# Optimization experiments

Measured on AMD Instinct MI355X. Metric: run time of the kernel, lower is better.

The kernel has to match this reference:

```python
import jax, jax.numpy as jnp
import numpy as np

B, L, E, H, A = 32, 4096, 512, 512, 256


def setup_inputs() -> dict:
    key = jax.random.key(0)
    ks = jax.random.split(key, 8)
    s_e = 1.0 / np.sqrt(E)
    s_h = 1.0 / np.sqrt(H)
    s_a = 1.0 / np.sqrt(A)
    return {
        "features": jax.random.normal(ks[0], (B, L, E), jnp.float32),
        "decoder_hidden": jax.random.normal(ks[1], (B, H), jnp.float32),
        "W_enc": jax.random.uniform(ks[2], (E, A), jnp.float32, -s_e, s_e),
        "b_enc": jax.random.uniform(ks[3], (A,), jnp.float32, -s_e, s_e),
        "W_dec": jax.random.uniform(ks[4], (H, A), jnp.float32, -s_h, s_h),
        "b_dec": jax.random.uniform(ks[5], (A,), jnp.float32, -s_h, s_h),
        "W_v": jax.random.uniform(ks[6], (A, 1), jnp.float32, -s_a, s_a),
        "b_v": jax.random.uniform(ks[7], (1,), jnp.float32, -s_a, s_a),
    }


def reference(features, decoder_hidden, W_enc, b_enc, W_dec, b_dec, W_v, b_v):
    # encoder/decoder projections
    enc_attn = jnp.einsum("ble,ea->bla", features, W_enc) + b_enc  # [B,L,A]
    dec_attn = decoder_hidden @ W_dec + b_dec                       # [B,A]
    sim = jax.nn.relu(enc_attn + dec_attn[:, None, :])              # [B,L,A]
    scores = (jnp.einsum("bla,ao->blo", sim, W_v) + b_v)[..., 0]    # [B,L]
    attn_weights = jax.nn.softmax(scores, axis=1)                   # [B,L]
    output = jnp.einsum("ble,bl->be", features, attn_weights)       # [B,E]
    return output, attn_weights
```

## Files before the change

kernel.cpp:

```cpp
#include <hip/hip_runtime.h>
#include <hip/hip_bf16.h>
#include <stdint.h>


typedef __attribute__((ext_vector_type(8))) short bf16x8;
typedef __attribute__((ext_vector_type(4))) float f32x4;

__device__ __forceinline__ unsigned short f32_to_bf16(float f) {
    union { float f; unsigned u; } v; v.f = f;
    unsigned u = v.u;
    u += 0x7fffu + ((u >> 16) & 1u);
    return (unsigned short)(u >> 16);
}

__device__ __forceinline__ void async_load16(const void* g, void* l) {
    __builtin_amdgcn_global_load_lds(
        (const __attribute__((address_space(1))) unsigned int*)g,
        (__attribute__((address_space(3))) unsigned int*)l, 16, 0, 0);
}

__global__ __launch_bounds__(256) void prep_kernel(
    const float* __restrict__ dh, const float* __restrict__ W_enc,
    const float* __restrict__ b_enc, const float* __restrict__ W_dec,
    const float* __restrict__ b_dec, unsigned short* __restrict__ Wp,
    float* __restrict__ dec_full, unsigned* __restrict__ cnt)
{
    int t = threadIdx.x;
    if (blockIdx.x < 32) {
        int b = blockIdx.x;
        if (b == 0 && t < 32) cnt[t] = 0;
        __shared__ float dhs[512];
        dhs[t]       = dh[b * 512 + t];
        dhs[t + 256] = dh[b * 512 + 256 + t];
        __syncthreads();
        float a0 = 0.f, a1 = 0.f, a2 = 0.f, a3 = 0.f;
        float a4 = 0.f, a5 = 0.f, a6 = 0.f, a7 = 0.f;
        #pragma unroll 4
        for (int h = 0; h < 512; h += 8) {
            a0 += dhs[h + 0] * W_dec[(h + 0) * 256 + t];
            a1 += dhs[h + 1] * W_dec[(h + 1) * 256 + t];
            a2 += dhs[h + 2] * W_dec[(h + 2) * 256 + t];
            a3 += dhs[h + 3] * W_dec[(h + 3) * 256 + t];
            a4 += dhs[h + 4] * W_dec[(h + 4) * 256 + t];
            a5 += dhs[h + 5] * W_dec[(h + 5) * 256 + t];
            a6 += dhs[h + 6] * W_dec[(h + 6) * 256 + t];
            a7 += dhs[h + 7] * W_dec[(h + 7) * 256 + t];
        }
        dec_full[b * 256 + t] =
            ((a0 + a1) + (a2 + a3)) + ((a4 + a5) + (a6 + a7)) + b_enc[t] + b_dec[t];
    } else {
        int tid = (blockIdx.x - 32) * 256 + t;
        #pragma unroll
        for (int i = 0; i < 8; ++i) {
            int d = tid + i * 16384;
            int j = d & 7;
            int n = (d >> 3) & 255;
            int chunk = (d >> 11) & 7;
            int kb = d >> 14;
            int k = kb * 64 + chunk * 8 + j;
            Wp[d] = f32_to_bf16(W_enc[k * 256 + n]);
        }
    }
}

__global__ __launch_bounds__(256, 2) void score_kernel(
    const float* __restrict__ feat, const unsigned short* __restrict__ Wp,
    const float* __restrict__ dec_full, const float* __restrict__ W_v,
    float* __restrict__ scores, float* __restrict__ m_c,
    float* __restrict__ o_part, unsigned* __restrict__ cnt,
    float* __restrict__ out)
{
    __shared__ unsigned short Alds[8192];
    __shared__ unsigned short Blds[16384];
    __shared__ float red[4][128];
    __shared__ float sblk[128];
    __shared__ float wexp[128];
    __shared__ float mshr;
    __shared__ float red2x[128], red2y[128], red2z[128], red2w[128];
    __shared__ unsigned dflag;

    const int t = threadIdx.x;
    const int lane = t & 63;
    const int wave = t >> 6;
    const int r0 = blockIdx.x * 128;
    const int b = r0 >> 12;

    float wv[4], dec[4];
    #pragma unroll
    for (int ct = 0; ct < 4; ++ct) {
        int a = wave * 64 + ct * 16 + (lane & 15);
        wv[ct] = W_v[a];
        dec[ct] = dec_full[b * 256 + a];
    }

    f32x4 acc[8][4];
    #pragma unroll
    for (int mt = 0; mt < 8; ++mt)
        #pragma unroll
        for (int ct = 0; ct < 4; ++ct)
            acc[mt][ct] = f32x4{0.f, 0.f, 0.f, 0.f};

    float4 av[8];
    #pragma unroll
    for (int it = 0; it < 8; ++it) {
        int lin = it * 256 + t;
        int m = lin >> 4, kq = lin & 15;
        av[it] = *(const float4*)(feat + (size_t)(r0 + m) * 512 + kq * 4);
    }

    for (int ks = 0; ks < 8; ++ks) {
        #pragma unroll
        for (int q = 0; q < 8; ++q) {
            int c = q * 256 + wave * 64 + lane;
            async_load16(Wp + ks * 16384 + c * 8, Blds + c * 8);
        }
        #pragma unroll
        for (int it = 0; it < 8; ++it) {
            int lin = it * 256 + t;
            int m = lin >> 4, kq = lin & 15;
            ushort4 w;
            w.x = f32_to_bf16(av[it].x);
            w.y = f32_to_bf16(av[it].y);
            w.z = f32_to_bf16(av[it].z);
            w.w = f32_to_bf16(av[it].w);
            int chunk = kq >> 1, jh = kq & 1;
            *(ushort4*)(Alds + m * 64 + ((chunk ^ (m & 7)) * 8) + jh * 4) = w;
        }
        __syncthreads();
        if (ks < 7) {
            #pragma unroll
            for (int it = 0; it < 8; ++it) {
                int lin = it * 256 + t;
                int m = lin >> 4, kq = lin & 15;
                av[it] = *(const float4*)(feat + (size_t)(r0 + m) * 512 + (ks + 1) * 64 + kq * 4);
            }
        }
        #pragma unroll
        for (int kk = 0; kk < 2; ++kk) {
            int chunk = kk * 4 + (lane >> 4);
            bf16x8 bfr[4];
            #pragma unroll
            for (int ct = 0; ct < 4; ++ct) {
                int n = wave * 64 + ct * 16 + (lane & 15);
                bfr[ct] = *(const bf16x8*)(Blds + (chunk * 256 + n) * 8);
            }
            #pragma unroll
            for (int mt = 0; mt < 8; ++mt) {
                int m = mt * 16 + (lane & 15);
                bf16x8 afr = *(const bf16x8*)(Alds + m * 64 + ((chunk ^ (m & 7)) * 8));
                #pragma unroll
                for (int ct = 0; ct < 4; ++ct)
                    acc[mt][ct] = __builtin_amdgcn_mfma_f32_16x16x32_bf16(
                        afr, bfr[ct], acc[mt][ct], 0, 0, 0);
            }
        }
        __syncthreads();
    }

    #pragma unroll
    for (int mt = 0; mt < 8; ++mt) {
        #pragma unroll
        for (int r = 0; r < 4; ++r) {
            float p = 0.f;
            #pragma unroll
            for (int ct = 0; ct < 4; ++ct) {
                float v = acc[mt][ct][r] + dec[ct];
                v = v > 0.f ? v : 0.f;
                p += v * wv[ct];
            }
            p += __shfl_xor(p, 1);
            p += __shfl_xor(p, 2);
            p += __shfl_xor(p, 4);
            p += __shfl_xor(p, 8);
            if ((lane & 15) == 0)
                red[wave][mt * 16 + (lane >> 4) * 4 + r] = p;
        }
    }
    __syncthreads();
    if (t < 128) {
        float v = red[0][t] + red[1][t] + red[2][t] + red[3][t];
        sblk[t] = v;
        scores[r0 + t] = v;
    }
    __syncthreads();
    if (t < 64) {
        float m = fmaxf(sblk[t], sblk[t + 64]);
        #pragma unroll
        for (int o = 1; o < 64; o <<= 1) m = fmaxf(m, __shfl_xor(m, o));
        if (t == 0) mshr = m;
    }
    __syncthreads();
    float mb = mshr;
    if (t < 128) wexp[t] = __expf(sblk[t] - mb);
    __syncthreads();

    int e4 = t & 127, lh = t >> 7;
    float ax = 0.f, ay = 0.f, az = 0.f, aw = 0.f;
    #pragma unroll 8
    for (int i = 0; i < 64; ++i) {
        int l = i * 2 + lh;
        float wl = wexp[l];
        const float4 f = *(const float4*)(feat + (size_t)(r0 + l) * 512 + e4 * 4);
        ax += wl * f.x; ay += wl * f.y; az += wl * f.z; aw += wl * f.w;
    }
    if (lh) { red2x[e4] = ax; red2y[e4] = ay; red2z[e4] = az; red2w[e4] = aw; }
    __syncthreads();
    if (!lh) {
        float4 r;
        r.x = ax + red2x[e4]; r.y = ay + red2y[e4];
        r.z = az + red2z[e4]; r.w = aw + red2w[e4];
        *(float4*)(o_part + (size_t)blockIdx.x * 512 + e4 * 4) = r;
        if (t == 0) m_c[blockIdx.x] = mb;
    }

    __syncthreads();
    if (t == 0) {
        unsigned old = __hip_atomic_fetch_add(cnt + b, 1u,
                                              __ATOMIC_ACQ_REL,
                                              __HIP_MEMORY_SCOPE_AGENT);
        dflag = (old == 31u) ? 1u : 0u;
    }
    __syncthreads();
    if (!dflag) return;

    const float* s = scores + b * 4096;
    float vals[16];
    float m = -1e30f;
    #pragma unroll
    for (int i = 0; i < 16; ++i) { vals[i] = s[t + i * 256]; m = fmaxf(m, vals[i]); }
    #pragma unroll
    for (int o = 1; o < 64; o <<= 1) m = fmaxf(m, __shfl_xor(m, o));
    if ((t & 63) == 0) red[0][t >> 6] = m;
    __syncthreads();
    m = fmaxf(fmaxf(red[0][0], red[0][1]), fmaxf(red[0][2], red[0][3]));

    float z = 0.f;
    #pragma unroll
    for (int i = 0; i < 16; ++i) { vals[i] = __expf(vals[i] - m); z += vals[i]; }
    #pragma unroll
    for (int o = 1; o < 64; o <<= 1) z += __shfl_xor(z, o);
    if ((t & 63) == 0) red[1][t >> 6] = z;
    __syncthreads();
    z = red[1][0] + red[1][1] + red[1][2] + red[1][3];
    float invz = 1.f / z;
    #pragma unroll
    for (int i = 0; i < 16; ++i)
        out[16384 + b * 4096 + t + i * 256] = vals[i] * invz;

    if (t < 32) red[2][t] = __expf(m_c[b * 32 + t] - m) * invz;
    __syncthreads();
    float a0 = 0.f, a1 = 0.f;
    #pragma unroll 8
    for (int c = 0; c < 32; ++c) {
        const float2 v = *(const float2*)(o_part + (size_t)(b * 32 + c) * 512 + t * 2);
        a0 += red[2][c] * v.x; a1 += red[2][c] * v.y;
    }
    float2 r2; r2.x = a0; r2.y = a1;
    *(float2*)(out + b * 512 + t * 2) = r2;
}

extern "C" void kernel_launch(void* const* d_in, const int* in_sizes, int n_in,
                              void* d_out, int out_size, void* d_ws, size_t ws_size,
                              hipStream_t stream) {
    const float* feat  = (const float*)d_in[0];
    const float* dh    = (const float*)d_in[1];
    const float* W_enc = (const float*)d_in[2];
    const float* b_enc = (const float*)d_in[3];
    const float* W_dec = (const float*)d_in[4];
    const float* b_dec = (const float*)d_in[5];
    const float* W_v   = (const float*)d_in[6];

    unsigned short* Wp = (unsigned short*)d_ws;
    float* dec_full = (float*)((char*)d_ws + 262144);
    float* scores   = (float*)((char*)d_ws + 294912);
    float* m_c      = (float*)((char*)d_ws + 819200);
    unsigned* cnt   = (unsigned*)((char*)d_ws + 823296);
    float* o_part   = (float*)((char*)d_ws + 1048576);
    float* out      = (float*)d_out;

    prep_kernel<<<96, 256, 0, stream>>>(dh, W_enc, b_enc, W_dec, b_dec, Wp, dec_full, cnt);
    score_kernel<<<1024, 256, 0, stream>>>(feat, Wp, dec_full, W_v, scores, m_c,
                                           o_part, cnt, out);
}
```

Measured before the change: 461.2 us.

## Halve row tile, read B fragments from global, double-buffer A in LDS

New measurement: 522.2 us. 13.2% more time.

```diff
diff --git a/kernel.cpp b/kernel.cpp
--- a/kernel.cpp
+++ b/kernel.cpp
@@ -11,12 +11,6 @@
     unsigned u = v.u;
     u += 0x7fffu + ((u >> 16) & 1u);
     return (unsigned short)(u >> 16);
-}
-
-__device__ __forceinline__ void async_load16(const void* g, void* l) {
-    __builtin_amdgcn_global_load_lds(
-        (const __attribute__((address_space(1))) unsigned int*)g,
-        (__attribute__((address_space(3))) unsigned int*)l, 16, 0, 0);
 }
 
 __global__ __launch_bounds__(256) void prep_kernel(
@@ -63,18 +57,17 @@
     }
 }
 
-__global__ __launch_bounds__(256, 2) void score_kernel(
+__global__ __launch_bounds__(256, 3) void score_kernel(
     const float* __restrict__ feat, const unsigned short* __restrict__ Wp,
     const float* __restrict__ dec_full, const float* __restrict__ W_v,
     float* __restrict__ scores, float* __restrict__ m_c,
     float* __restrict__ o_part, unsigned* __restrict__ cnt,
     float* __restrict__ out)
 {
-    __shared__ unsigned short Alds[8192];
-    __shared__ unsigned short Blds[16384];
-    __shared__ float red[4][128];
-    __shared__ float sblk[128];
-    __shared__ float wexp[128];
+    __shared__ __align__(16) unsigned short Alds[2][4096];
+    __shared__ float red[4][64];
+    __shared__ float sblk[64];
+    __shared__ float wexp[64];
     __shared__ float mshr;
     __shared__ float red2x[128], red2y[128], red2z[128], red2w[128];
     __shared__ unsigned dflag;
@@ -82,7 +75,7 @@
     const int t = threadIdx.x;
     const int lane = t & 63;
     const int wave = t >> 6;
-    const int r0 = blockIdx.x * 128;
+    const int r0 = blockIdx.x * 64;
     const int b = r0 >> 12;
 
     float wv[4], dec[4];
@@ -93,48 +86,45 @@
         dec[ct] = dec_full[b * 256 + a];
     }
 
-    f32x4 acc[8][4];
-    #pragma unroll
-    for (int mt = 0; mt < 8; ++mt)
+    f32x4 acc[4][4];
+    #pragma unroll
+    for (int mt = 0; mt < 4; ++mt)
         #pragma unroll
         for (int ct = 0; ct < 4; ++ct)
             acc[mt][ct] = f32x4{0.f, 0.f, 0.f, 0.f};
 
-    float4 av[8];
-    #pragma unroll
-    for (int it = 0; it < 8; ++it) {
+    float4 av[4];
+    #pragma unroll
+    for (int it = 0; it < 4; ++it) {
         int lin = it * 256 + t;
         int m = lin >> 4, kq = lin & 15;
         av[it] = *(const float4*)(feat + (size_t)(r0 + m) * 512 + kq * 4);
     }
+    #pragma unroll
+    for (int it = 0; it < 4; ++it) {
+        int lin = it * 256 + t;
+        int m = lin >> 4, kq = lin & 15;
+        ushort4 w;
+        w.x = f32_to_bf16(av[it].x);
+        w.y = f32_to_bf16(av[it].y);
+        w.z = f32_to_bf16(av[it].z);
+        w.w = f32_to_bf16(av[it].w);
+        int chunk = kq >> 1, jh = kq & 1;
+        *(ushort4*)(&Alds[0][m * 64 + ((chunk ^ (m & 7)) * 8) + jh * 4]) = w;
+    }
+    __syncthreads();
 
     for (int ks = 0; ks < 8; ++ks) {
-        #pragma unroll
-        for (int q = 0; q < 8; ++q) {
-            int c = q * 256 + wave * 64 + lane;
-            async_load16(Wp + ks * 16384 + c * 8, Blds + c * 8);
-        }
-        #pragma unroll
-        for (int it = 0; it < 8; ++it) {
-            int lin = it * 256 + t;
-            int m = lin >> 4, kq = lin & 15;
-            ushort4 w;
-            w.x = f32_to_bf16(av[it].x);
-            w.y = f32_to_bf16(av[it].y);
-            w.z = f32_to_bf16(av[it].z);
-            w.w = f32_to_bf16(av[it].w);
-            int chunk = kq >> 1, jh = kq & 1;
-            *(ushort4*)(Alds + m * 64 + ((chunk ^ (m & 7)) * 8) + jh * 4) = w;
-        }
-        __syncthreads();
+        const int cur = ks & 1;
         if (ks < 7) {
             #pragma unroll
-            for (int it = 0; it < 8; ++it) {
+            for (int it = 0; it < 4; ++it) {
                 int lin = it * 256 + t;
                 int m = lin >> 4, kq = lin & 15;
                 av[it] = *(const float4*)(feat + (size_t)(r0 + m) * 512 + (ks + 1) * 64 + kq * 4);
             }
         }
+        const unsigned short* Bp = Wp + ks * 16384;
         #pragma unroll
         for (int kk = 0; kk < 2; ++kk) {
             int chunk = kk * 4 + (lane >> 4);
@@ -142,23 +132,37 @@
             #pragma unroll
             for (int ct = 0; ct < 4; ++ct) {
                 int n = wave * 64 + ct * 16 + (lane & 15);
-                bfr[ct] = *(const bf16x8*)(Blds + (chunk * 256 + n) * 8);
-            }
-            #pragma unroll
-            for (int mt = 0; mt < 8; ++mt) {
+                bfr[ct] = *(const bf16x8*)(Bp + (chunk * 256 + n) * 8);
+            }
+            #pragma unroll
+            for (int mt = 0; mt < 4; ++mt) {
                 int m = mt * 16 + (lane & 15);
-                bf16x8 afr = *(const bf16x8*)(Alds + m * 64 + ((chunk ^ (m & 7)) * 8));
+                bf16x8 afr = *(const bf16x8*)(&Alds[cur][m * 64 + ((chunk ^ (m & 7)) * 8)]);
                 #pragma unroll
                 for (int ct = 0; ct < 4; ++ct)
                     acc[mt][ct] = __builtin_amdgcn_mfma_f32_16x16x32_bf16(
                         afr, bfr[ct], acc[mt][ct], 0, 0, 0);
             }
         }
+        if (ks < 7) {
+            #pragma unroll
+            for (int it = 0; it < 4; ++it) {
+                int lin = it * 256 + t;
+                int m = lin >> 4, kq = lin & 15;
+                ushort4 w;
+                w.x = f32_to_bf16(av[it].x);
+                w.y = f32_to_bf16(av[it].y);
+                w.z = f32_to_bf16(av[it].z);
+                w.w = f32_to_bf16(av[it].w);
+                int chunk = kq >> 1, jh = kq & 1;
+                *(ushort4*)(&Alds[cur ^ 1][m * 64 + ((chunk ^ (m & 7)) * 8) + jh * 4]) = w;
+            }
+        }
         __syncthreads();
     }
 
     #pragma unroll
-    for (int mt = 0; mt < 8; ++mt) {
+    for (int mt = 0; mt < 4; ++mt) {
         #pragma unroll
         for (int r = 0; r < 4; ++r) {
             float p = 0.f;
@@ -177,27 +181,24 @@
         }
     }
     __syncthreads();
-    if (t < 128) {
+    if (t < 64) {
         float v = red[0][t] + red[1][t] + red[2][t] + red[3][t];
         sblk[t] = v;
         scores[r0 + t] = v;
-    }
-    __syncthreads();
-    if (t < 64) {
-        float m = fmaxf(sblk[t], sblk[t + 64]);
+        float m = v;
         #pragma unroll
         for (int o = 1; o < 64; o <<= 1) m = fmaxf(m, __shfl_xor(m, o));
         if (t == 0) mshr = m;
     }
     __syncthreads();
     float mb = mshr;
-    if (t < 128) wexp[t] = __expf(sblk[t] - mb);
+    if (t < 64) wexp[t] = __expf(sblk[t] - mb);
     __syncthreads();
 
     int e4 = t & 127, lh = t >> 7;
     float ax = 0.f, ay = 0.f, az = 0.f, aw = 0.f;
     #pragma unroll 8
-    for (int i = 0; i < 64; ++i) {
+    for (int i = 0; i < 32; ++i) {
         int l = i * 2 + lh;
         float wl = wexp[l];
         const float4 f = *(const float4*)(feat + (size_t)(r0 + l) * 512 + e4 * 4);
@@ -218,7 +219,7 @@
         unsigned old = __hip_atomic_fetch_add(cnt + b, 1u,
                                               __ATOMIC_ACQ_REL,
                                               __HIP_MEMORY_SCOPE_AGENT);
-        dflag = (old == 31u) ? 1u : 0u;
+        dflag = (old == 63u) ? 1u : 0u;
     }
     __syncthreads();
     if (!dflag) return;
@@ -247,13 +248,13 @@
     for (int i = 0; i < 16; ++i)
         out[16384 + b * 4096 + t + i * 256] = vals[i] * invz;
 
-    if (t < 32) red[2][t] = __expf(m_c[b * 32 + t] - m) * invz;
+    if (t < 64) wexp[t] = __expf(m_c[b * 64 + t] - m) * invz;
     __syncthreads();
     float a0 = 0.f, a1 = 0.f;
     #pragma unroll 8
-    for (int c = 0; c < 32; ++c) {
-        const float2 v = *(const float2*)(o_part + (size_t)(b * 32 + c) * 512 + t * 2);
-        a0 += red[2][c] * v.x; a1 += red[2][c] * v.y;
+    for (int c = 0; c < 64; ++c) {
+        const float2 v = *(const float2*)(o_part + (size_t)(b * 64 + c) * 512 + t * 2);
+        a0 += wexp[c] * v.x; a1 += wexp[c] * v.y;
     }
     float2 r2; r2.x = a0; r2.y = a1;
     *(float2*)(out + b * 512 + t * 2) = r2;
@@ -274,11 +275,11 @@
     float* dec_full = (float*)((char*)d_ws + 262144);
     float* scores   = (float*)((char*)d_ws + 294912);
     float* m_c      = (float*)((char*)d_ws + 819200);
-    unsigned* cnt   = (unsigned*)((char*)d_ws + 823296);
+    unsigned* cnt   = (unsigned*)((char*)d_ws + 827392);
     float* o_part   = (float*)((char*)d_ws + 1048576);
     float* out      = (float*)d_out;
 
     prep_kernel<<<96, 256, 0, stream>>>(dh, W_enc, b_enc, W_dec, b_dec, Wp, dec_full, cnt);
-    score_kernel<<<1024, 256, 0, stream>>>(feat, Wp, dec_full, W_v, scores, m_c,
+    score_kernel<<<2048, 256, 0, stream>>>(feat, Wp, dec_full, W_v, scores, m_c,
                                            o_part, cnt, out);
 }
```
